# Optimization experiments

Hardware: AMD Instinct MI355X
Metric: run time of the kernel (lower is better)

## Reference

```python
import jax, jax.numpy as jnp
import numpy as np

ALPHA = 0.2  # LeakyReLU negative slope


def setup_inputs() -> dict:
    key = jax.random.key(0)
    k1, k2, k3 = jax.random.split(key, 3)
    B, N, IN, OUT = 64, 2048, 1024, 1024
    features = jax.random.normal(k1, (B, N, IN), dtype=jnp.float32)
    # Xavier-uniform-ish scaling for weights
    W = jax.random.normal(k2, (OUT, IN), dtype=jnp.float32) * (1.0 / np.sqrt(IN))
    w_b = jnp.zeros((OUT,), dtype=jnp.float32)
    a_w = jax.random.normal(k3, (2 * OUT,), dtype=jnp.float32) * (1.0 / np.sqrt(2 * OUT))
    a_b = jnp.zeros((), dtype=jnp.float32)
    bias_out = jnp.zeros((OUT,), dtype=jnp.float32)
    return {"features": features, "W": W, "w_b": w_b, "a_w": a_w, "a_b": a_b, "bias_out": bias_out}


def reference(features, W, w_b, a_w, a_b, bias_out):
    # h = Linear(in_dim, out_dim)(features): [B, N, D]
    h = jnp.einsum('bni,di->bnd', features, W) + w_b
    D = h.shape[-1]
    a1, a2 = a_w[:D], a_w[D:]
    # concat([h_expand, h]) @ a == h[:, :1] . a1 + h . a2  (h_expand broadcasts node 0)
    e = (h[:, 0:1, :] @ a1[:, None]) + jnp.einsum('bnd,d->bn', h, a2)[..., None] + a_b  # [B, N, 1]
    e = jnp.where(e >= 0, e, ALPHA * e)  # LeakyReLU
    attention = jax.nn.softmax(e, axis=1)  # softmax over nodes, [B, N, 1]
    # dropout p=0.0 -> identity
    pooled = jnp.einsum('bnk,bnd->bkd', attention, h)  # [B, 1, D]
    return jax.nn.relu(pooled + bias_out)
```

## Files before the change

kernel.cpp:

```cpp
#include <hip/hip_runtime.h>

#define ALPHA 0.2f
constexpr int B_   = 64;
constexpr int N_   = 2048;
constexpr int IN_  = 1024;
constexpr int OUT_ = 1024;
constexpr int CHUNK = 128;
constexpr int NCH   = N_ / CHUNK;
constexpr int RPW   = CHUNK / 4;

constexpr size_t WA1   = 0;
constexpr size_t WA2   = 1024;
constexpr size_t E0    = 2048;
constexpr size_t ZPART = 2112;
constexpr size_t PART1 = 4096;
constexpr size_t PART2 = 135168;
constexpr size_t GPART = 270336;
constexpr size_t GV    = 1318912;

__device__ inline float wave_reduce_sum(float v) {
    #pragma unroll
    for (int off = 32; off > 0; off >>= 1) v += __shfl_xor(v, off);
    return v;
}

__global__ void kA1(const float* __restrict__ W, const float* __restrict__ aw,
                    float* __restrict__ ws) {
    int t = threadIdx.x, blk = blockIdx.x;
    float4 acc1 = make_float4(0.f, 0.f, 0.f, 0.f);
    float4 acc2 = make_float4(0.f, 0.f, 0.f, 0.f);
    #pragma unroll
    for (int r = 0; r < 8; ++r) {
        int d = blk * 8 + r;
        float a1 = aw[d], a2 = aw[OUT_ + d];
        float4 w = ((const float4*)(W + (size_t)d * IN_))[t];
        acc1.x += a1 * w.x; acc1.y += a1 * w.y; acc1.z += a1 * w.z; acc1.w += a1 * w.w;
        acc2.x += a2 * w.x; acc2.y += a2 * w.y; acc2.z += a2 * w.z; acc2.w += a2 * w.w;
    }
    ((float4*)(ws + PART1))[blk * 256 + t] = acc1;
    ((float4*)(ws + PART2))[blk * 256 + t] = acc2;
}

__global__ void kA2(float* __restrict__ ws) {
    int idx = blockIdx.x * 256 + threadIdx.x;
    int which = idx >> 10, col = idx & 1023;
    const float* p = ws + (which ? PART2 : PART1) + col;
    float s = 0.f;
    #pragma unroll 8
    for (int r = 0; r < 128; ++r) s += p[(size_t)r * 1024];
    ws[(which ? WA2 : WA1) + col] = s;
}

__global__ void kP(const float* __restrict__ f, const float* __restrict__ wb,
                   const float* __restrict__ aw, float* __restrict__ ws) {
    int b = blockIdx.x, t = threadIdx.x;
    float4 v   = ((const float4*)(f + (size_t)b * N_ * IN_))[t];
    float4 w1  = ((const float4*)(ws + WA1))[t];
    float4 wbv = ((const float4*)wb)[t];
    float4 a1v = ((const float4*)aw)[t];
    float4 a2v = ((const float4*)(aw + OUT_))[t];
    float p = v.x * w1.x + v.y * w1.y + v.z * w1.z + v.w * w1.w
            + wbv.x * (a1v.x + a2v.x) + wbv.y * (a1v.y + a2v.y)
            + wbv.z * (a1v.z + a2v.z) + wbv.w * (a1v.w + a2v.w);
    __shared__ float red[256];
    red[t] = p;
    __syncthreads();
    for (int off = 128; off > 0; off >>= 1) {
        if (t < off) red[t] += red[t + off];
        __syncthreads();
    }
    if (t == 0) ws[E0 + b] = red[0];
}

__global__ void kMain(const float* __restrict__ f, const float* __restrict__ ab,
                      float* __restrict__ ws) {
    int b = blockIdx.y, chunk = blockIdx.x;
    int t = threadIdx.x, wave = t >> 6, lane = t & 63;
    float cst = ws[E0 + b] + ab[0];

    const float4* wa2_4 = (const float4*)(ws + WA2);
    float4 ra2[4];
    #pragma unroll
    for (int k = 0; k < 4; ++k) ra2[k] = wa2_4[k * 64 + lane];

    const float4* fbase = (const float4*)(f + ((size_t)b * N_ + (size_t)chunk * CHUNK) * IN_);
    float4 acc[4];
    #pragma unroll
    for (int k = 0; k < 4; ++k) acc[k] = make_float4(0.f, 0.f, 0.f, 0.f);
    float z = 0.f;

    float4 v[4], nv[4];
    int r = wave;
    #pragma unroll
    for (int k = 0; k < 4; ++k) v[k] = fbase[(size_t)r * 256 + k * 64 + lane];

    for (int i = 0; i < RPW; ++i) {
        int rn = r + 4;
        if (i + 1 < RPW) {
            #pragma unroll
            for (int k = 0; k < 4; ++k) nv[k] = fbase[(size_t)rn * 256 + k * 64 + lane];
        }
        float dot = 0.f;
        #pragma unroll
        for (int k = 0; k < 4; ++k)
            dot += v[k].x * ra2[k].x + v[k].y * ra2[k].y + v[k].z * ra2[k].z + v[k].w * ra2[k].w;
        dot = wave_reduce_sum(dot);
        float e = dot + cst;
        e = e >= 0.f ? e : ALPHA * e;
        float w = __expf(e);
        z += w;
        #pragma unroll
        for (int k = 0; k < 4; ++k) {
            acc[k].x += w * v[k].x; acc[k].y += w * v[k].y;
            acc[k].z += w * v[k].z; acc[k].w += w * v[k].w;
        }
        if (i + 1 < RPW) {
            #pragma unroll
            for (int k = 0; k < 4; ++k) v[k] = nv[k];
        }
        r = rn;
    }

    __shared__ float4 gbuf[4][256];
    __shared__ float  zbuf[4];
    #pragma unroll
    for (int k = 0; k < 4; ++k) gbuf[wave][k * 64 + lane] = acc[k];
    if (lane == 0) zbuf[wave] = z;
    __syncthreads();
    float4 s0 = gbuf[0][t], s1 = gbuf[1][t], s2 = gbuf[2][t], s3 = gbuf[3][t];
    float4 s = make_float4(s0.x + s1.x + s2.x + s3.x, s0.y + s1.y + s2.y + s3.y,
                           s0.z + s1.z + s2.z + s3.z, s0.w + s1.w + s2.w + s3.w);
    ((float4*)(ws + GPART))[((size_t)b * NCH + chunk) * 256 + t] = s;
    if (t == 0) ws[ZPART + b * NCH + chunk] = zbuf[0] + zbuf[1] + zbuf[2] + zbuf[3];
}

__global__ void kE(float* __restrict__ ws) {
    int b = blockIdx.x, t = threadIdx.x;
    __shared__ float zinv;
    if (t == 0) {
        float zz = 0.f;
        #pragma unroll
        for (int c = 0; c < NCH; ++c) zz += ws[ZPART + b * NCH + c];
        zinv = 1.0f / zz;
    }
    __syncthreads();
    const float4* gp = (const float4*)(ws + GPART);
    float4 acc = make_float4(0.f, 0.f, 0.f, 0.f);
    #pragma unroll
    for (int c = 0; c < NCH; ++c) {
        float4 v = gp[((size_t)b * NCH + c) * 256 + t];
        acc.x += v.x; acc.y += v.y; acc.z += v.z; acc.w += v.w;
    }
    acc.x *= zinv; acc.y *= zinv; acc.z *= zinv; acc.w *= zinv;
    ((float4*)(ws + GV))[b * 256 + t] = acc;
}

__global__ void kF(const float* __restrict__ W, const float* __restrict__ wb,
                   const float* __restrict__ bias, const float* __restrict__ ws,
                   float* __restrict__ out) {
    int t = threadIdx.x, wave = t >> 6, lane = t & 63;
    int d = blockIdx.x * 4 + wave;
    const float4* w4 = (const float4*)(W + (size_t)d * IN_);
    float4 wreg[4];
    #pragma unroll
    for (int k = 0; k < 4; ++k) wreg[k] = w4[k * 64 + lane];
    float wbb = wb[d] + bias[d];
    const float4* gv = (const float4*)(ws + GV);
    #pragma unroll 4
    for (int b = 0; b < B_; ++b) {
        float acc = 0.f;
        #pragma unroll
        for (int k = 0; k < 4; ++k) {
            float4 g = gv[b * 256 + k * 64 + lane];
            acc += g.x * wreg[k].x + g.y * wreg[k].y + g.z * wreg[k].z + g.w * wreg[k].w;
        }
        acc = wave_reduce_sum(acc);
        if (lane == 0) {
            float p = acc + wbb;
            out[(size_t)b * OUT_ + d] = p > 0.f ? p : 0.f;
        }
    }
}

extern "C" void kernel_launch(void* const* d_in, const int* in_sizes, int n_in,
                              void* d_out, int out_size, void* d_ws, size_t ws_size,
                              hipStream_t stream) {
    const float* f    = (const float*)d_in[0];
    const float* W    = (const float*)d_in[1];
    const float* wb   = (const float*)d_in[2];
    const float* aw   = (const float*)d_in[3];
    const float* ab   = (const float*)d_in[4];
    const float* bias = (const float*)d_in[5];
    float* out = (float*)d_out;
    float* ws  = (float*)d_ws;

    kA1<<<dim3(128), 256, 0, stream>>>(W, aw, ws);
    kA2<<<dim3(8), 256, 0, stream>>>(ws);
    kP <<<dim3(B_), 256, 0, stream>>>(f, wb, aw, ws);
    kMain<<<dim3(NCH, B_), 256, 0, stream>>>(f, ab, ws);
    kE <<<dim3(B_), 256, 0, stream>>>(ws);
    kF <<<dim3(OUT_ / 4), 256, 0, stream>>>(W, wb, bias, ws, out);
}
```

Before: 148.8 us.

## Merge weight-reduction and node-0 score kernels, double chunk size, split output GEMV over batch

The separate kA2 reduction and kP node-0 score kernels become one launch. The score blocks compute the node-0 dot product straight from the 128 partial rows of W^T a1, so they no longer wait for the reduced vector. kMain now processes 256 rows per block instead of 128, which halves the partial-sum traffic and the kE reduction work but also halves the grid to 512 blocks. kF is split over two batch halves to double its block count. Together these cut one kernel launch and shorten the small serial kernels, at the cost of less parallelism in the main streaming kernel.

```diff
diff --git a/kernel.cpp b/kernel.cpp
--- a/kernel.cpp
+++ b/kernel.cpp
@@ -5,7 +5,7 @@
 constexpr int N_   = 2048;
 constexpr int IN_  = 1024;
 constexpr int OUT_ = 1024;
-constexpr int CHUNK = 128;
+constexpr int CHUNK = 256;
 constexpr int NCH   = N_ / CHUNK;
 constexpr int RPW   = CHUNK / 4;
 
@@ -15,8 +15,8 @@
 constexpr size_t ZPART = 2112;
 constexpr size_t PART1 = 4096;
 constexpr size_t PART2 = 135168;
-constexpr size_t GPART = 270336;
-constexpr size_t GV    = 1318912;
+constexpr size_t GPART = 266240;
+constexpr size_t GV    = 790528;
 
 __device__ inline float wave_reduce_sum(float v) {
     #pragma unroll
@@ -24,8 +24,8 @@
     return v;
 }
 
-__global__ void kA1(const float* __restrict__ W, const float* __restrict__ aw,
-                    float* __restrict__ ws) {
+__global__ void kW(const float* __restrict__ W, const float* __restrict__ aw,
+                   float* __restrict__ ws) {
     int t = threadIdx.x, blk = blockIdx.x;
     float4 acc1 = make_float4(0.f, 0.f, 0.f, 0.f);
     float4 acc2 = make_float4(0.f, 0.f, 0.f, 0.f);
@@ -41,35 +41,41 @@
     ((float4*)(ws + PART2))[blk * 256 + t] = acc2;
 }
 
-__global__ void kA2(float* __restrict__ ws) {
-    int idx = blockIdx.x * 256 + threadIdx.x;
-    int which = idx >> 10, col = idx & 1023;
-    const float* p = ws + (which ? PART2 : PART1) + col;
-    float s = 0.f;
-    #pragma unroll 8
-    for (int r = 0; r < 128; ++r) s += p[(size_t)r * 1024];
-    ws[(which ? WA2 : WA1) + col] = s;
-}
-
-__global__ void kP(const float* __restrict__ f, const float* __restrict__ wb,
+__global__ void kS(const float* __restrict__ f, const float* __restrict__ wb,
                    const float* __restrict__ aw, float* __restrict__ ws) {
-    int b = blockIdx.x, t = threadIdx.x;
-    float4 v   = ((const float4*)(f + (size_t)b * N_ * IN_))[t];
-    float4 w1  = ((const float4*)(ws + WA1))[t];
-    float4 wbv = ((const float4*)wb)[t];
-    float4 a1v = ((const float4*)aw)[t];
-    float4 a2v = ((const float4*)(aw + OUT_))[t];
-    float p = v.x * w1.x + v.y * w1.y + v.z * w1.z + v.w * w1.w
-            + wbv.x * (a1v.x + a2v.x) + wbv.y * (a1v.y + a2v.y)
-            + wbv.z * (a1v.z + a2v.z) + wbv.w * (a1v.w + a2v.w);
-    __shared__ float red[256];
-    red[t] = p;
-    __syncthreads();
-    for (int off = 128; off > 0; off >>= 1) {
-        if (t < off) red[t] += red[t + off];
+    int t = threadIdx.x;
+    if (blockIdx.x < 8) {
+        int idx = blockIdx.x * 256 + t;
+        int which = idx >> 10, col = idx & 1023;
+        const float* p = ws + (which ? PART2 : PART1) + col;
+        float s = 0.f;
+        #pragma unroll 8
+        for (int r = 0; r < 128; ++r) s += p[(size_t)r * 1024];
+        ws[(which ? WA2 : WA1) + col] = s;
+    } else {
+        int b = blockIdx.x - 8;
+        float4 fv = ((const float4*)(f + (size_t)b * N_ * IN_))[t];
+        const float4* p1 = (const float4*)(ws + PART1);
+        float acc = 0.f;
+        #pragma unroll 8
+        for (int r = 0; r < 128; ++r) {
+            float4 p = p1[(size_t)r * 256 + t];
+            acc += fv.x * p.x + fv.y * p.y + fv.z * p.z + fv.w * p.w;
+        }
+        float4 wbv = ((const float4*)wb)[t];
+        float4 a1v = ((const float4*)aw)[t];
+        float4 a2v = ((const float4*)(aw + OUT_))[t];
+        acc += wbv.x * (a1v.x + a2v.x) + wbv.y * (a1v.y + a2v.y)
+             + wbv.z * (a1v.z + a2v.z) + wbv.w * (a1v.w + a2v.w);
+        __shared__ float red[256];
+        red[t] = acc;
         __syncthreads();
-    }
-    if (t == 0) ws[E0 + b] = red[0];
+        for (int off = 128; off > 0; off >>= 1) {
+            if (t < off) red[t] += red[t + off];
+            __syncthreads();
+        }
+        if (t == 0) ws[E0 + b] = red[0];
+    }
 }
 
 __global__ void kMain(const float* __restrict__ f, const float* __restrict__ ab,
@@ -159,7 +165,8 @@
                    const float* __restrict__ bias, const float* __restrict__ ws,
                    float* __restrict__ out) {
     int t = threadIdx.x, wave = t >> 6, lane = t & 63;
-    int d = blockIdx.x * 4 + wave;
+    int d  = blockIdx.x * 4 + wave;
+    int b0 = blockIdx.y * 32;
     const float4* w4 = (const float4*)(W + (size_t)d * IN_);
     float4 wreg[4];
     #pragma unroll
@@ -167,7 +174,8 @@
     float wbb = wb[d] + bias[d];
     const float4* gv = (const float4*)(ws + GV);
     #pragma unroll 4
-    for (int b = 0; b < B_; ++b) {
+    for (int bi = 0; bi < 32; ++bi) {
+        int b = b0 + bi;
         float acc = 0.f;
         #pragma unroll
         for (int k = 0; k < 4; ++k) {
@@ -194,10 +202,9 @@
     float* out = (float*)d_out;
     float* ws  = (float*)d_ws;
 
-    kA1<<<dim3(128), 256, 0, stream>>>(W, aw, ws);
-    kA2<<<dim3(8), 256, 0, stream>>>(ws);
-    kP <<<dim3(B_), 256, 0, stream>>>(f, wb, aw, ws);
+    kW   <<<dim3(128), 256, 0, stream>>>(W, aw, ws);
+    kS   <<<dim3(8 + B_), 256, 0, stream>>>(f, wb, aw, ws);
     kMain<<<dim3(NCH, B_), 256, 0, stream>>>(f, ab, ws);
-    kE <<<dim3(B_), 256, 0, stream>>>(ws);
-    kF <<<dim3(OUT_ / 4), 256, 0, stream>>>(W, wb, bias, ws, out);
-}
+    kE   <<<dim3(B_), 256, 0, stream>>>(ws);
+    kF   <<<dim3(OUT_ / 4, 2), 256, 0, stream>>>(W, wb, bias, ws, out);
+}
```

After: 129.8 us. 1.15x faster.
